# Optimization experiments

Hardware: AMD Instinct MI355X
Metric: run time of the kernel (lower is better)

The kernel has to match this reference:

```python
import jax, jax.numpy as jnp
import numpy as np


def setup_inputs() -> dict:
    key = jax.random.key(0)
    k1, k2, k3 = jax.random.split(key, 3)
    B, N_old, N_new, F = 8, 2048, 4096, 256
    X = jax.random.normal(k1, (B, N_old, F), dtype=jnp.float32)
    A = jax.random.uniform(k2, (B, N_new, N_new), dtype=jnp.float32)
    idx = jax.random.randint(k3, (B, N_old, 1), 0, N_new, dtype=jnp.int32)
    return {"X": X, "A": A, "idx": idx}


def reference(X, A, idx):
    # X: [B, N_old, F]; A: [B, N_new, N_new]; idx: [B, N_old, 1]
    B, N_old, F = X.shape
    N_new = A.shape[1]
    node_idx = idx.reshape(B, N_old)  # [B, N_old]
    batch_idx = jnp.arange(B, dtype=node_idx.dtype)[:, None]  # [B, 1]
    # tf.scatter_nd sums duplicate indices into a zero buffer -> use .at[].add
    new_X = jnp.zeros((B, N_new, F), dtype=X.dtype).at[batch_idx, node_idx].add(X)
    return (new_X, A)
```

## Files before the change

kernel.cpp:

```cpp
#include <hip/hip_runtime.h>


typedef float f32x4 __attribute__((ext_vector_type(4)));

constexpr int B_     = 8;
constexpr int N_OLD  = 2048;
constexpr int N_NEW  = 4096;
constexpr int F_     = 256;

constexpr int ROWS_IN   = B_ * N_OLD;
constexpr int ROWS_OUT  = B_ * N_NEW;
constexpr size_t NEWX_ELEMS = (size_t)ROWS_OUT * F_;
constexpr size_t A_ELEMS    = (size_t)B_ * N_NEW * (size_t)N_NEW;
constexpr size_t A_VEC4     = A_ELEMS / 4;

constexpr int CAP = 32;
constexpr size_t COUNTS_BYTES  = (size_t)ROWS_OUT * sizeof(int);
constexpr size_t ENTRIES_BYTES = (size_t)ROWS_OUT * CAP * sizeof(int);
constexpr size_t WS_NEEDED     = COUNTS_BYTES + ENTRIES_BYTES;

constexpr int GATHER_BLOCKS = ROWS_OUT / 4;
constexpr int COPY_BLOCKS   = 8192;


__global__ void build_index_kernel(const int* __restrict__ idx,
                                   int* __restrict__ counts,
                                   int* __restrict__ entries) {
    const int i = blockIdx.x * blockDim.x + threadIdx.x;
    const int b = i >> 11;
    const int node = idx[i];
    const int bin = (b << 12) + node;
    const int pos = atomicAdd(&counts[bin], 1);
    if (pos < CAP) entries[bin * CAP + pos] = i;
}

__global__ void fused_gather_copy_kernel(const f32x4* __restrict__ X4,
                                         const f32x4* __restrict__ A4,
                                         const int* __restrict__ counts,
                                         const int* __restrict__ entries,
                                         f32x4* __restrict__ newX4,
                                         f32x4* __restrict__ Aout4) {
    if (blockIdx.x < GATHER_BLOCKS) {
        const int wave = threadIdx.x >> 6;
        const int lane = threadIdx.x & 63;
        const int row  = blockIdx.x * 4 + wave;
        int c = counts[row];
        if (c > CAP) c = CAP;
        f32x4 acc = (f32x4)(0.f);
        const int* e = &entries[(size_t)row * CAP];
        for (int k = 0; k < c; ++k) {
            const int src = e[k];
            acc += X4[(size_t)src * 64 + lane];
        }
        newX4[(size_t)row * 64 + lane] = acc;
    } else {
        size_t tid = (size_t)(blockIdx.x - GATHER_BLOCKS) * blockDim.x + threadIdx.x;
        const size_t stride = (size_t)COPY_BLOCKS * 256;
        for (size_t i = tid; i < A_VEC4; i += stride) {
            const f32x4 v = __builtin_nontemporal_load(&A4[i]);
            __builtin_nontemporal_store(v, &Aout4[i]);
        }
    }
}


__global__ void zero_newx_kernel(float4* __restrict__ p, size_t n4) {
    size_t i = (size_t)blockIdx.x * blockDim.x + threadIdx.x;
    size_t stride = (size_t)gridDim.x * blockDim.x;
    const float4 z = make_float4(0.f, 0.f, 0.f, 0.f);
    for (; i < n4; i += stride) p[i] = z;
}

__global__ void scatter_add_kernel(const float* __restrict__ X,
                                   const int* __restrict__ idx,
                                   float* __restrict__ out) {
    const int row = blockIdx.x;
    const int f   = threadIdx.x;
    const int b   = row / N_OLD;
    const int node = idx[row];
    const float v = X[(size_t)row * F_ + f];
    atomicAdd(&out[((size_t)b * N_NEW + node) * (size_t)F_ + f], v);
}

extern "C" void kernel_launch(void* const* d_in, const int* in_sizes, int n_in,
                              void* d_out, int out_size, void* d_ws, size_t ws_size,
                              hipStream_t stream) {
    const float* X   = (const float*)d_in[0];
    const float* A   = (const float*)d_in[1];
    const int*   idx = (const int*)d_in[2];

    float* newX  = (float*)d_out;
    float* A_out = (float*)d_out + NEWX_ELEMS;

    if (ws_size >= WS_NEEDED) {
        int* counts  = (int*)d_ws;
        int* entries = (int*)((char*)d_ws + COUNTS_BYTES);

        (void)hipMemsetAsync(counts, 0, COUNTS_BYTES, stream);

        build_index_kernel<<<ROWS_IN / 256, 256, 0, stream>>>(idx, counts, entries);

        fused_gather_copy_kernel<<<GATHER_BLOCKS + COPY_BLOCKS, 256, 0, stream>>>(
            (const f32x4*)X, (const f32x4*)A, counts, entries,
            (f32x4*)newX, (f32x4*)A_out);
    } else {
        zero_newx_kernel<<<2048, 256, 0, stream>>>((float4*)newX, NEWX_ELEMS / 4);
        scatter_add_kernel<<<ROWS_IN, 256, 0, stream>>>(X, idx, newX);
        (void)hipMemcpyAsync(A_out, A, A_ELEMS * sizeof(float),
                             hipMemcpyDeviceToDevice, stream);
    }
}
```

Measured before the change: 217.0 us.

## Merge gather and A-copy roles into every block with prefetched copy loads

Every block now does both jobs, where before separate blocks handled either the gather or the copy. Each block gathers its four output rows and also copies a strided slice of A. The first four A loads are issued before the gather so their latency overlaps the gather's random X reads. The copy loop is fixed-trip and unrolled by four, and the newX store becomes nontemporal. This drops the block divergence and the extra gather-only blocks, but it relies on the compile-time iteration count dividing evenly and raises register pressure.

New measurement: 223.8 us. 3.1% more time.

```diff
diff --git a/kernel.cpp b/kernel.cpp
--- a/kernel.cpp
+++ b/kernel.cpp
@@ -19,8 +19,9 @@
 constexpr size_t ENTRIES_BYTES = (size_t)ROWS_OUT * CAP * sizeof(int);
 constexpr size_t WS_NEEDED     = COUNTS_BYTES + ENTRIES_BYTES;
 
-constexpr int GATHER_BLOCKS = ROWS_OUT / 4;
-constexpr int COPY_BLOCKS   = 8192;
+constexpr int    BLOCKS = 8192;
+constexpr size_t STRIDE = (size_t)BLOCKS * 256;
+constexpr int    ITERS  = (int)(A_VEC4 / STRIDE);
 
 
 __global__ void build_index_kernel(const int* __restrict__ idx,
@@ -28,38 +29,56 @@
                                    int* __restrict__ entries) {
     const int i = blockIdx.x * blockDim.x + threadIdx.x;
     const int b = i >> 11;
-    const int node = idx[i];
-    const int bin = (b << 12) + node;
+    const int bin = (b << 12) + idx[i];
     const int pos = atomicAdd(&counts[bin], 1);
     if (pos < CAP) entries[bin * CAP + pos] = i;
 }
 
-__global__ void fused_gather_copy_kernel(const f32x4* __restrict__ X4,
-                                         const f32x4* __restrict__ A4,
-                                         const int* __restrict__ counts,
-                                         const int* __restrict__ entries,
-                                         f32x4* __restrict__ newX4,
-                                         f32x4* __restrict__ Aout4) {
-    if (blockIdx.x < GATHER_BLOCKS) {
-        const int wave = threadIdx.x >> 6;
-        const int lane = threadIdx.x & 63;
-        const int row  = blockIdx.x * 4 + wave;
-        int c = counts[row];
-        if (c > CAP) c = CAP;
-        f32x4 acc = (f32x4)(0.f);
-        const int* e = &entries[(size_t)row * CAP];
-        for (int k = 0; k < c; ++k) {
-            const int src = e[k];
-            acc += X4[(size_t)src * 64 + lane];
-        }
-        newX4[(size_t)row * 64 + lane] = acc;
-    } else {
-        size_t tid = (size_t)(blockIdx.x - GATHER_BLOCKS) * blockDim.x + threadIdx.x;
-        const size_t stride = (size_t)COPY_BLOCKS * 256;
-        for (size_t i = tid; i < A_VEC4; i += stride) {
-            const f32x4 v = __builtin_nontemporal_load(&A4[i]);
-            __builtin_nontemporal_store(v, &Aout4[i]);
-        }
+
+__global__ __launch_bounds__(256) void fused_gather_copy_kernel(
+        const f32x4* __restrict__ X4,
+        const f32x4* __restrict__ A4,
+        const int*   __restrict__ counts,
+        const int*   __restrict__ entries,
+        f32x4* __restrict__ newX4,
+        f32x4* __restrict__ Aout4) {
+    const int wave = threadIdx.x >> 6;
+    const int lane = threadIdx.x & 63;
+    const int row  = blockIdx.x * 4 + wave;
+
+    size_t i = (size_t)blockIdx.x * 256 + threadIdx.x;
+
+    f32x4 v0 = __builtin_nontemporal_load(&A4[i]);
+    f32x4 v1 = __builtin_nontemporal_load(&A4[i +     STRIDE]);
+    f32x4 v2 = __builtin_nontemporal_load(&A4[i + 2 * STRIDE]);
+    f32x4 v3 = __builtin_nontemporal_load(&A4[i + 3 * STRIDE]);
+
+    int c = counts[row];
+    if (c > CAP) c = CAP;
+    f32x4 acc = (f32x4)(0.f);
+    const int* e = &entries[(size_t)row * CAP];
+    for (int k = 0; k < c; ++k) {
+        acc += X4[(size_t)e[k] * 64 + lane];
+    }
+    __builtin_nontemporal_store(acc, &newX4[(size_t)row * 64 + lane]);
+
+    __builtin_nontemporal_store(v0, &Aout4[i]);
+    __builtin_nontemporal_store(v1, &Aout4[i +     STRIDE]);
+    __builtin_nontemporal_store(v2, &Aout4[i + 2 * STRIDE]);
+    __builtin_nontemporal_store(v3, &Aout4[i + 3 * STRIDE]);
+    i += 4 * STRIDE;
+
+    #pragma unroll
+    for (int it = 1; it < ITERS / 4; ++it) {
+        f32x4 w0 = __builtin_nontemporal_load(&A4[i]);
+        f32x4 w1 = __builtin_nontemporal_load(&A4[i +     STRIDE]);
+        f32x4 w2 = __builtin_nontemporal_load(&A4[i + 2 * STRIDE]);
+        f32x4 w3 = __builtin_nontemporal_load(&A4[i + 3 * STRIDE]);
+        __builtin_nontemporal_store(w0, &Aout4[i]);
+        __builtin_nontemporal_store(w1, &Aout4[i +     STRIDE]);
+        __builtin_nontemporal_store(w2, &Aout4[i + 2 * STRIDE]);
+        __builtin_nontemporal_store(w3, &Aout4[i + 3 * STRIDE]);
+        i += 4 * STRIDE;
     }
 }
 
@@ -100,7 +119,7 @@
 
         build_index_kernel<<<ROWS_IN / 256, 256, 0, stream>>>(idx, counts, entries);
 
-        fused_gather_copy_kernel<<<GATHER_BLOCKS + COPY_BLOCKS, 256, 0, stream>>>(
+        fused_gather_copy_kernel<<<BLOCKS, 256, 0, stream>>>(
             (const f32x4*)X, (const f32x4*)A, counts, entries,
             (f32x4*)newX, (f32x4*)A_out);
     } else {
```

## Interleave gather and copy blocks in the fused kernel, four rows per wave

Applied to the files above, without the earlier changes.

Changes the fused kernel's work split so that every eighth block does the scatter-gather and the other seven copy A. Gather and copy traffic are therefore interleaved across the grid instead of running as two sequential phases. Each gather wave now handles four output rows, and newX is written with nontemporal stores. The copy loop is unrolled by two over a fixed stride. The aim is better overlap of the irregular gather with the streaming copy. The risk is load imbalance: there are fewer gather blocks, and each does more work.

Result: faster. 202.6 us (-6.6%).

```diff
diff --git a/kernel.cpp b/kernel.cpp
--- a/kernel.cpp
+++ b/kernel.cpp
@@ -19,8 +19,10 @@
 constexpr size_t ENTRIES_BYTES = (size_t)ROWS_OUT * CAP * sizeof(int);
 constexpr size_t WS_NEEDED     = COUNTS_BYTES + ENTRIES_BYTES;
 
-constexpr int GATHER_BLOCKS = ROWS_OUT / 4;
-constexpr int COPY_BLOCKS   = 8192;
+constexpr int TOTAL_BLOCKS  = 16384;
+constexpr int GATHER_BLOCKS = TOTAL_BLOCKS / 8;
+constexpr int COPY_BLOCKS   = TOTAL_BLOCKS - GATHER_BLOCKS;
+constexpr size_t COPY_STRIDE = (size_t)COPY_BLOCKS * 256;
 
 
 __global__ void build_index_kernel(const int* __restrict__ idx,
@@ -28,35 +30,40 @@
                                    int* __restrict__ entries) {
     const int i = blockIdx.x * blockDim.x + threadIdx.x;
     const int b = i >> 11;
-    const int node = idx[i];
-    const int bin = (b << 12) + node;
+    const int bin = (b << 12) + idx[i];
     const int pos = atomicAdd(&counts[bin], 1);
     if (pos < CAP) entries[bin * CAP + pos] = i;
 }
 
-__global__ void fused_gather_copy_kernel(const f32x4* __restrict__ X4,
-                                         const f32x4* __restrict__ A4,
-                                         const int* __restrict__ counts,
-                                         const int* __restrict__ entries,
-                                         f32x4* __restrict__ newX4,
-                                         f32x4* __restrict__ Aout4) {
-    if (blockIdx.x < GATHER_BLOCKS) {
+
+__global__ __launch_bounds__(256) void fused_gather_copy_kernel(
+        const f32x4* __restrict__ X4,
+        const f32x4* __restrict__ A4,
+        const int*   __restrict__ counts,
+        const int*   __restrict__ entries,
+        f32x4* __restrict__ newX4,
+        f32x4* __restrict__ Aout4) {
+    const int j = blockIdx.x & 7;
+    if (j == 0) {
+        const int gid  = blockIdx.x >> 3;
         const int wave = threadIdx.x >> 6;
         const int lane = threadIdx.x & 63;
-        const int row  = blockIdx.x * 4 + wave;
-        int c = counts[row];
-        if (c > CAP) c = CAP;
-        f32x4 acc = (f32x4)(0.f);
-        const int* e = &entries[(size_t)row * CAP];
-        for (int k = 0; k < c; ++k) {
-            const int src = e[k];
-            acc += X4[(size_t)src * 64 + lane];
+        #pragma unroll
+        for (int r = 0; r < 4; ++r) {
+            const int row = gid * 16 + wave * 4 + r;
+            int c = counts[row];
+            if (c > CAP) c = CAP;
+            f32x4 acc = (f32x4)(0.f);
+            const int* e = &entries[(size_t)row * CAP];
+            for (int k = 0; k < c; ++k)
+                acc += X4[(size_t)e[k] * 64 + lane];
+            __builtin_nontemporal_store(acc, &newX4[(size_t)row * 64 + lane]);
         }
-        newX4[(size_t)row * 64 + lane] = acc;
     } else {
-        size_t tid = (size_t)(blockIdx.x - GATHER_BLOCKS) * blockDim.x + threadIdx.x;
-        const size_t stride = (size_t)COPY_BLOCKS * 256;
-        for (size_t i = tid; i < A_VEC4; i += stride) {
+        const size_t cid = (size_t)(blockIdx.x >> 3) * 7 + (j - 1);
+        size_t i = cid * 256 + threadIdx.x;
+        #pragma unroll 2
+        for (; i < A_VEC4; i += COPY_STRIDE) {
             const f32x4 v = __builtin_nontemporal_load(&A4[i]);
             __builtin_nontemporal_store(v, &Aout4[i]);
         }
@@ -100,7 +107,7 @@
 
         build_index_kernel<<<ROWS_IN / 256, 256, 0, stream>>>(idx, counts, entries);
 
-        fused_gather_copy_kernel<<<GATHER_BLOCKS + COPY_BLOCKS, 256, 0, stream>>>(
+        fused_gather_copy_kernel<<<TOTAL_BLOCKS, 256, 0, stream>>>(
             (const f32x4*)X, (const f32x4*)A, counts, entries,
             (f32x4*)newX, (f32x4*)A_out);
     } else {
```
